# Optimization experiments

Measured on AMD Instinct MI355X. Metric: run time of the kernel, lower is better.

The kernel has to match this reference:

```python
import jax, jax.numpy as jnp
import numpy as np

B, T, F, H, L = 2048, 200, 64, 128, 1  # batch, train_window, input feat, hidden, encoder_layers


def setup_inputs() -> dict:
    key = jax.random.key(0)
    ks = jax.random.split(key, 6)
    s = 1.0 / np.sqrt(H)  # PyTorch LSTMCell init range
    return {
        "encode_features": jax.random.normal(ks[0], (B, T, F), dtype=jnp.float32),
        "x_len": jax.random.randint(ks[1], (B,), 0, T),
        "W_ih": jax.random.uniform(ks[2], (4 * H, F), jnp.float32, -s, s),
        "W_hh": jax.random.uniform(ks[3], (4 * H, H), jnp.float32, -s, s),
        "b_ih": jax.random.uniform(ks[4], (4 * H,), jnp.float32, -s, s),
        "b_hh": jax.random.uniform(ks[5], (4 * H,), jnp.float32, -s, s),
    }


def _lstm_cell(x, h, c, W_ih, W_hh, b_ih, b_hh):
    # x: [B,T,F], h/c: [B,T,H]; the original applies nn.LSTMCell with T as the
    # cell's batch dim, one call per batch element -> fully vectorizable.
    gates = jnp.einsum('btf,gf->btg', x, W_ih) + b_ih \
          + jnp.einsum('bth,gh->btg', h, W_hh) + b_hh
    i, f, g, o = jnp.split(gates, 4, axis=-1)  # PyTorch gate order: i,f,g,o
    c_new = jax.nn.sigmoid(f) * c + jax.nn.sigmoid(i) * jnp.tanh(g)
    h_new = jax.nn.sigmoid(o) * jnp.tanh(c_new)
    return h_new, c_new


def reference(encode_features, x_len, W_ih, W_hh, b_ih, b_hh):
    Bb, Tt, _ = encode_features.shape
    # index = x_len - 1, clamped to 0 when x_len == 0
    index = jnp.where(x_len == 0, jnp.zeros_like(x_len), x_len - 1)
    h = jnp.zeros((Bb, Tt, H), dtype=encode_features.dtype)
    c = jnp.zeros((Bb, Tt, H), dtype=encode_features.dtype)
    rows = jnp.arange(Bb)
    hs, cs = [], []
    for _ in range(L):  # all layers share one cell's weights (as in source)
        h, c = _lstm_cell(encode_features, h, c, W_ih, W_hh, b_ih, b_hh)
        hs.append(h[rows, index])  # [B,H] gather at last valid timestep
        cs.append(c[rows, index])
    return jnp.stack(hs), jnp.stack(cs)  # each [L,B,H]
```

## Files before the change

### kernel.cpp

```cpp
#include <hip/hip_runtime.h>


namespace {
constexpr int Bc = 2048;
constexpr int Tc = 200;
constexpr int Fc = 64;
constexpr int Hc = 128;
constexpr int TF = Tc * Fc;
constexpr int ROWS_PER_BLOCK = 8;
}

__global__ __launch_bounds__(256, 1)
void lstm_last_step_kernel(const float* __restrict__ x,
                           const int*   __restrict__ xlen,
                           const float* __restrict__ W,
                           const float* __restrict__ b_ih,
                           const float* __restrict__ b_hh,
                           float*       __restrict__ out)
{
  const int t = threadIdx.x;
  const int j = t & (Hc - 1);
  const int r = t >> 7;
  const int b0 = blockIdx.x * ROWS_PER_BLOCK;

  float4 wi[16], wg[16], wo[16];
  const float4* W4 = reinterpret_cast<const float4*>(W);
  #pragma unroll
  for (int q = 0; q < 16; ++q) {
    wi[q] = W4[(0 * Hc + j) * 16 + q];
    wg[q] = W4[(2 * Hc + j) * 16 + q];
    wo[q] = W4[(3 * Hc + j) * 16 + q];
  }
  const float bi = b_ih[0 * Hc + j] + b_hh[0 * Hc + j];
  const float bg = b_ih[2 * Hc + j] + b_hh[2 * Hc + j];
  const float bo = b_ih[3 * Hc + j] + b_hh[3 * Hc + j];

  __shared__ float xs[ROWS_PER_BLOCK][Fc];
  #pragma unroll
  for (int k = 0; k < 2; ++k) {
    const int lin = t + 256 * k;
    const int rr  = lin >> 6;
    const int f   = lin & 63;
    const int b   = b0 + rr;
    const int len = xlen[b];
    const int idx = (len == 0) ? 0 : (len - 1);
    xs[rr][f] = x[b * TF + idx * Fc + f];
  }
  __syncthreads();

  #pragma unroll
  for (int p = 0; p < 4; ++p) {
    const int rowlocal = p * 2 + r;
    const int b = b0 + rowlocal;
    const float4* xv = reinterpret_cast<const float4*>(xs[rowlocal]);

    float ai = bi, ag = bg, ao = bo;
    #pragma unroll
    for (int q = 0; q < 16; ++q) {
      const float4 xq = xv[q];
      ai = fmaf(wi[q].x, xq.x, ai);
      ai = fmaf(wi[q].y, xq.y, ai);
      ai = fmaf(wi[q].z, xq.z, ai);
      ai = fmaf(wi[q].w, xq.w, ai);
      ag = fmaf(wg[q].x, xq.x, ag);
      ag = fmaf(wg[q].y, xq.y, ag);
      ag = fmaf(wg[q].z, xq.z, ag);
      ag = fmaf(wg[q].w, xq.w, ag);
      ao = fmaf(wo[q].x, xq.x, ao);
      ao = fmaf(wo[q].y, xq.y, ao);
      ao = fmaf(wo[q].z, xq.z, ao);
      ao = fmaf(wo[q].w, xq.w, ao);
    }

    const float si = 1.0f / (1.0f + expf(-ai));
    const float so = 1.0f / (1.0f + expf(-ao));
    const float tg = tanhf(ag);
    const float c  = si * tg;
    const float h  = so * tanhf(c);

    out[b * Hc + j]           = h;
    out[Bc * Hc + b * Hc + j] = c;
  }
}

extern "C" void kernel_launch(void* const* d_in, const int* in_sizes, int n_in,
                              void* d_out, int out_size, void* d_ws, size_t ws_size,
                              hipStream_t stream) {
  const float* x     = (const float*)d_in[0];
  const int*   xlen  = (const int*)  d_in[1];
  const float* W_ih  = (const float*)d_in[2];
  const float* b_ih  = (const float*)d_in[4];
  const float* b_hh  = (const float*)d_in[5];
  float*       out   = (float*)d_out;

  lstm_last_step_kernel<<<Bc / ROWS_PER_BLOCK, 256, 0, stream>>>(
      x, xlen, W_ih, b_ih, b_hh, out);
}
```

Measured before the change: 145.2 us.

## Use 128-thread blocks over two batch rows, issue x gather before weight loads

Each block now runs 128 threads and handles two batch rows, so the grid grows from 256 to 1024 blocks and more CUs get work. The gather of the last-valid-timestep x row is issued before the weight register loads so the two memory latencies overlap. Sigmoid switches to the fast __expf intrinsic. The trade-off is that each block reloads the gate weights into registers for fewer rows, which adds redundant weight traffic, though it should mostly hit cache.

```diff
diff --git a/kernel.cpp b/kernel.cpp
--- a/kernel.cpp
+++ b/kernel.cpp
@@ -7,10 +7,10 @@
 constexpr int Fc = 64;
 constexpr int Hc = 128;
 constexpr int TF = Tc * Fc;
-constexpr int ROWS_PER_BLOCK = 8;
+constexpr int R  = 2;
 }
 
-__global__ __launch_bounds__(256, 1)
+__global__ __launch_bounds__(128, 2)
 void lstm_last_step_kernel(const float* __restrict__ x,
                            const int*   __restrict__ xlen,
                            const float* __restrict__ W,
@@ -18,10 +18,18 @@
                            const float* __restrict__ b_hh,
                            float*       __restrict__ out)
 {
-  const int t = threadIdx.x;
-  const int j = t & (Hc - 1);
-  const int r = t >> 7;
-  const int b0 = blockIdx.x * ROWS_PER_BLOCK;
+  const int j  = threadIdx.x;
+  const int b0 = blockIdx.x * R;
+
+  __shared__ float xs[R][Fc];
+  {
+    const int rr = j >> 6;
+    const int f  = j & 63;
+    const int b  = b0 + rr;
+    const int len = xlen[b];
+    const int idx = (len == 0) ? 0 : (len - 1);
+    xs[rr][f] = x[b * TF + idx * Fc + f];
+  }
 
   float4 wi[16], wg[16], wo[16];
   const float4* W4 = reinterpret_cast<const float4*>(W);
@@ -35,24 +43,12 @@
   const float bg = b_ih[2 * Hc + j] + b_hh[2 * Hc + j];
   const float bo = b_ih[3 * Hc + j] + b_hh[3 * Hc + j];
 
-  __shared__ float xs[ROWS_PER_BLOCK][Fc];
-  #pragma unroll
-  for (int k = 0; k < 2; ++k) {
-    const int lin = t + 256 * k;
-    const int rr  = lin >> 6;
-    const int f   = lin & 63;
-    const int b   = b0 + rr;
-    const int len = xlen[b];
-    const int idx = (len == 0) ? 0 : (len - 1);
-    xs[rr][f] = x[b * TF + idx * Fc + f];
-  }
   __syncthreads();
 
   #pragma unroll
-  for (int p = 0; p < 4; ++p) {
-    const int rowlocal = p * 2 + r;
-    const int b = b0 + rowlocal;
-    const float4* xv = reinterpret_cast<const float4*>(xs[rowlocal]);
+  for (int rr = 0; rr < R; ++rr) {
+    const int b = b0 + rr;
+    const float4* xv = reinterpret_cast<const float4*>(xs[rr]);
 
     float ai = bi, ag = bg, ao = bo;
     #pragma unroll
@@ -72,8 +68,8 @@
       ao = fmaf(wo[q].w, xq.w, ao);
     }
 
-    const float si = 1.0f / (1.0f + expf(-ai));
-    const float so = 1.0f / (1.0f + expf(-ao));
+    const float si = 1.0f / (1.0f + __expf(-ai));
+    const float so = 1.0f / (1.0f + __expf(-ao));
     const float tg = tanhf(ag);
     const float c  = si * tg;
     const float h  = so * tanhf(c);
@@ -86,13 +82,12 @@
 extern "C" void kernel_launch(void* const* d_in, const int* in_sizes, int n_in,
                               void* d_out, int out_size, void* d_ws, size_t ws_size,
                               hipStream_t stream) {
-  const float* x     = (const float*)d_in[0];
-  const int*   xlen  = (const int*)  d_in[1];
-  const float* W_ih  = (const float*)d_in[2];
-  const float* b_ih  = (const float*)d_in[4];
-  const float* b_hh  = (const float*)d_in[5];
-  float*       out   = (float*)d_out;
+  const float* x    = (const float*)d_in[0];
+  const int*   xlen = (const int*)  d_in[1];
+  const float* W_ih = (const float*)d_in[2];
+  const float* b_ih = (const float*)d_in[4];
+  const float* b_hh = (const float*)d_in[5];
+  float*       out  = (float*)d_out;
 
-  lstm_last_step_kernel<<<Bc / ROWS_PER_BLOCK, 256, 0, stream>>>(
-      x, xlen, W_ih, b_ih, b_hh, out);
+  lstm_last_step_kernel<<<Bc / R, 128, 0, stream>>>(x, xlen, W_ih, b_ih, b_hh, out);
 }
```

Result: slower. 152.5 us (+5.1%).
